# Performance work log

Measured on AMD Instinct MI355X. Metric: run time of the kernel, lower is better.

The kernel has to match this reference:

```python
import jax, jax.numpy as jnp
import numpy as np

# Problem dimensions (match init_kwargs / input_specs)
B, NT = 4, 256          # shots, timesteps
NZ, NX = 384, 384       # domain
NREC = 128              # receivers
DT, DH = 0.001, 10.0    # time step [s], grid spacing [m]


def setup_inputs() -> dict:
    key = jax.random.key(0)
    k1, k2, k3, k4, k5, k6 = jax.random.split(key, 6)
    # source wavelets, one per shot: [B, NT]
    x = jax.random.normal(k1, (B, NT), dtype=jnp.float32)
    # velocity model 1500..3500 m/s: [NZ, NX]
    vp = 1500.0 + 2000.0 * jax.random.uniform(k2, (NZ, NX), dtype=jnp.float32)
    # per-shot source locations (kept away from the boundary)
    src_y = jax.random.randint(k3, (B,), 20, NZ - 20, dtype=jnp.int32)
    src_x = jax.random.randint(k4, (B,), 20, NX - 20, dtype=jnp.int32)
    # shared receiver array
    rec_y = jax.random.randint(k5, (NREC,), 20, NZ - 20, dtype=jnp.int32)
    rec_x = jax.random.randint(k6, (NREC,), 20, NX - 20, dtype=jnp.int32)
    return {"x": x, "vp": vp, "src_y": src_y, "src_x": src_x,
            "rec_y": rec_y, "rec_x": rec_x}


def _laplacian(u, inv_dh2):
    # 5-point stencil with zero (Dirichlet) boundaries; u: [B, NZ, NX]
    l = (u[:, 2:, 1:-1] + u[:, :-2, 1:-1]
         + u[:, 1:-1, 2:] + u[:, 1:-1, :-2]
         - 4.0 * u[:, 1:-1, 1:-1]) * inv_dh2
    return jnp.pad(l, ((0, 0), (1, 1), (1, 1)))


def reference(x, vp, src_y, src_x, rec_y, rec_x):
    """Second-order acoustic wave time-stepping with scatter source injection
    and receiver gather, as in WaveRNN.forward. Returns [NT, B, NREC] traces."""
    c2dt2 = (vp * DT) ** 2            # [NZ, NX], broadcast over shots
    inv_dh2 = jnp.float32(1.0 / (DH * DH))
    bidx = jnp.arange(B)

    def step(carry, xt):
        h1, h2 = carry                # current / previous wavefields [B,NZ,NX]
        hn = 2.0 * h1 - h2 + c2dt2 * _laplacian(h1, inv_dh2)
        hn = hn.at[bidx, src_y, src_x].add(xt)   # source injection (smask scatter)
        rec = hn[:, rec_y, rec_x]                 # receiver gather [B, NREC]
        return (hn, h1), rec

    h0 = jnp.zeros((B, NZ, NX), dtype=x.dtype)
    (_, _), y = jax.lax.scan(jax.checkpoint(step), (h0, h0), x.T)  # scan over time
    return y  # [NT, B, NREC]
```

## Files before the change

kernel.cpp:

```cpp
#include <hip/hip_runtime.h>

#define BB 4
#define NT 256
#define NZ 384
#define NX 384
#define NREC 128
#define NZX (NZ*NX)
#define BNZX (BB*NZX)
#define DT 0.001f
#define INV_DH2 0.01f

#define TILE 48
#define HALO 8
#define REGN 64
#define NBLK 256
#define NTHR 512
#define FSTRIDE 16

__global__ void wave_init(unsigned* flags) {
    int i = blockIdx.x * blockDim.x + threadIdx.x;
    if (i < NBLK * FSTRIDE) flags[i] = 0u;
}

__device__ inline float dpp_shl1(float v) {
    return __int_as_float(__builtin_amdgcn_update_dpp(
        0, __float_as_int(v), 0x130 , 0xf, 0xf, true));
}
__device__ inline float dpp_shr1(float v) {
    return __int_as_float(__builtin_amdgcn_update_dpp(
        0, __float_as_int(v), 0x138 , 0xf, 0xf, true));
}

__device__ inline void grid_sync(unsigned* flags, unsigned gen, int nbId) {
    __syncthreads();
    if (threadIdx.x < 64) {
        if (threadIdx.x == 0)
            __hip_atomic_store(&flags[blockIdx.x * FSTRIDE], gen,
                               __ATOMIC_RELAXED, __HIP_MEMORY_SCOPE_AGENT);
        for (;;) {
            unsigned f = __hip_atomic_load(&flags[nbId * FSTRIDE],
                             __ATOMIC_RELAXED, __HIP_MEMORY_SCOPE_AGENT);
            if (__all(f >= gen)) break;
            __builtin_amdgcn_s_sleep(1);
        }
    }
    __syncthreads();
}

__global__ __launch_bounds__(NTHR)
void wave_tiled(float* __restrict__ ws, const float* __restrict__ vp,
                const float* __restrict__ x,
                const int* __restrict__ src_y, const int* __restrict__ src_x,
                const int* __restrict__ rec_y, const int* __restrict__ rec_x,
                float* __restrict__ y) {
    __shared__ float bnd[2][16][REGN];
    __shared__ float recBuf[NREC][8];
    __shared__ float xs[NT];
    __shared__ int recLoc[NREC], recOut[NREC];
    __shared__ int recCnt;

    unsigned* flags = (unsigned*)(ws + 4*BNZX);

    const int tid = threadIdx.x;
    const int col = tid & 63;
    const int w   = tid >> 6;
    const int r0  = w << 3;
    const int blk = blockIdx.x;
    const int b  = blk >> 6;
    const int tz = (blk >> 3) & 7;
    const int tx = blk & 7;
    const int oz = tz*TILE - HALO, ox = tx*TILE - HALO;
    const int gx = ox + col;
    const int sy = src_y[b], sx = src_x[b];

    if (tid == 0) recCnt = 0;
    for (int k = tid; k < 16*REGN; k += NTHR) ((float*)bnd[0])[k] = 0.f;
    for (int k = tid; k < NT; k += NTHR) xs[k] = x[b*NT + k];
    __syncthreads();
    for (int r = tid; r < NREC; r += NTHR) {
        int ry = rec_y[r], rx = rec_x[r];
        if (ry/TILE == tz && rx/TILE == tx) {
            int p = atomicAdd(&recCnt, 1);
            recLoc[p] = ((ry - oz) << 6) | (rx - ox);
            recOut[p] = b*NREC + r;
        }
    }
    __syncthreads();

    int myN = 0, myM[4], myP[4];
    bool ovf = false;
    for (int p = 0; p < recCnt; ++p) {
        int rl = recLoc[p];
        if ((rl & 63) == col) {
            int rm = (rl >> 6) - r0;
            if ((unsigned)rm < 8u) {
                if (myN < 4) { myM[myN] = rm; myP[myN] = p; ++myN; }
                else ovf = true;
            }
        }
    }

    int nbId = blk;
    if (tid < 8) {
        int d = tid + (tid >= 4);
        int nz2 = tz + d/3 - 1, nx2 = tx + d%3 - 1;
        if ((unsigned)nz2 < 8u && (unsigned)nx2 < 8u)
            nbId = (b << 6) | (nz2 << 3) | nx2;
    }

    float cur[8], prv[8], c2i[8];
    #pragma unroll
    for (int m = 0; m < 8; ++m) {
        cur[m] = 0.f; prv[m] = 0.f;
        const int gz = oz + r0 + m;
        const bool inner = (gz > 0 && gz < NZ-1 && gx > 0 && gx < NX-1);
        const float v = inner ? vp[gz*NX + gx] * DT : 0.f;
        c2i[m] = v * v * INV_DH2;
    }
    const bool srcCol = (gx == sx);
    const int  srcM   = sy - oz - r0;
    const int  iuUp   = (2*w-1 < 0) ? 0 : 2*w-1;
    const int  iuDn   = (2*w+2 > 15) ? 15 : 2*w+2;
    __syncthreads();

    #pragma unroll 1
    for (int t = 0; t < NT; ++t) {
        const int pr = t & 1, pw = pr ^ 1;
        const float upB = bnd[pr][iuUp][col];
        const float dnB = bnd[pr][iuDn][col];

        float hn[8];
        #pragma unroll
        for (int m = 0; m < 8; ++m) {
            const float ce = cur[m];
            const float up = (m == 0) ? upB : cur[m-1];
            const float dn = (m == 7) ? dnB : cur[m+1];
            const float lf = dpp_shl1(ce);
            const float rt = dpp_shr1(ce);
            const float s  = (up + dn) + (lf + rt);
            hn[m] = fmaf(2.f, ce, -prv[m]) + c2i[m] * fmaf(-4.f, ce, s);
        }
        #pragma unroll
        for (int m = 0; m < 8; ++m) { prv[m] = cur[m]; cur[m] = hn[m]; }

        if (srcCol && (unsigned)srcM < 8u) {
            const float xv = xs[t];
            #pragma unroll
            for (int m = 0; m < 8; ++m) if (m == srcM) cur[m] += xv;
        }
        {
            const int s2 = t & 7;
            if (ovf) {
                for (int p = 0; p < recCnt; ++p) {
                    int rl = recLoc[p];
                    if ((rl & 63) == col) {
                        int rm = (rl >> 6) - r0;
                        if ((unsigned)rm < 8u) {
                            float v = cur[0];
                            #pragma unroll
                            for (int m = 1; m < 8; ++m) if (rm == m) v = cur[m];
                            recBuf[p][s2] = v;
                        }
                    }
                }
            } else {
                #pragma unroll
                for (int k = 0; k < 4; ++k) {
                    if (k < myN) {
                        float v = cur[0];
                        #pragma unroll
                        for (int m = 1; m < 8; ++m) if (myM[k] == m) v = cur[m];
                        recBuf[myP[k]][s2] = v;
                    }
                }
            }
        }
        bnd[pw][2*w  ][col] = cur[0];
        bnd[pw][2*w+1][col] = cur[7];

        if ((t & 7) == 7) {
            const int o = t >> 3;
            __syncthreads();
            for (int k = tid; k < recCnt*8; k += NTHR) {
                int p = k >> 3, s2 = k & 7;
                y[(size_t)((o<<3)+s2)*(BB*NREC) + recOut[p]] = recBuf[p][s2];
            }
            if (t < NT-1) {
                float* Gc = ws + (size_t)(o & 1) * 2*BNZX;
                float* Gp = Gc + BNZX;
                const bool colF = (col >= HALO   && col < REGN-HALO);
                const bool colM = (col >= 2*HALO && col < REGN-2*HALO);
                #pragma unroll
                for (int m = 0; m < 8; ++m) {
                    const int i = r0 + m;
                    const bool rowF = (i >= HALO   && i < REGN-HALO);
                    const bool rowM = (i >= 2*HALO && i < REGN-2*HALO);
                    if (colF && rowF && !(colM && rowM)) {
                        const size_t g = (size_t)b*NZX + (size_t)(oz+i)*NX + gx;
                        __hip_atomic_store(&Gc[g], cur[m],
                                           __ATOMIC_RELAXED, __HIP_MEMORY_SCOPE_AGENT);
                        __hip_atomic_store(&Gp[g], prv[m],
                                           __ATOMIC_RELAXED, __HIP_MEMORY_SCOPE_AGENT);
                    }
                }
                grid_sync(flags, (unsigned)(o + 1), nbId);
                const bool colH = (col < HALO || col >= REGN-HALO);
                const bool gxIn = (gx >= 0 && gx < NX);
                #pragma unroll
                for (int m = 0; m < 8; ++m) {
                    const int i = r0 + m;
                    if (colH || i < HALO || i >= REGN-HALO) {
                        const int gz = oz + i;
                        if (gxIn && gz >= 0 && gz < NZ) {
                            const size_t g = (size_t)b*NZX + (size_t)gz*NX + gx;
                            cur[m] = __hip_atomic_load(&Gc[g],
                                         __ATOMIC_RELAXED, __HIP_MEMORY_SCOPE_AGENT);
                            prv[m] = __hip_atomic_load(&Gp[g],
                                         __ATOMIC_RELAXED, __HIP_MEMORY_SCOPE_AGENT);
                        } else { cur[m] = 0.f; prv[m] = 0.f; }
                    }
                }
                bnd[pw][2*w  ][col] = cur[0];
                bnd[pw][2*w+1][col] = cur[7];
            }
        }
        __syncthreads();
    }
}

extern "C" void kernel_launch(void* const* d_in, const int* in_sizes, int n_in,
                              void* d_out, int out_size, void* d_ws, size_t ws_size,
                              hipStream_t stream) {
    const float* x     = (const float*)d_in[0];
    const float* vp    = (const float*)d_in[1];
    const int*   src_y = (const int*)d_in[2];
    const int*   src_x = (const int*)d_in[3];
    const int*   rec_y = (const int*)d_in[4];
    const int*   rec_x = (const int*)d_in[5];
    float* y  = (float*)d_out;
    float* ws = (float*)d_ws;

    wave_init<<<(NBLK*FSTRIDE + 255)/256, 256, 0, stream>>>((unsigned*)(ws + 4*BNZX));
    wave_tiled<<<NBLK, NTHR, 0, stream>>>(ws, vp, x, src_y, src_x, rec_y, rec_x, y);
}
```

Before: 273.0 us.

## Use 16-step halo with 32-wide tiles to halve grid syncs, pack cur/prv

Widens the halo to 16 and shrinks tile interiors to 32, so 576 blocks (12x12 tiles per shot) exchange halos and grid-sync every 16 steps instead of every 8. The edge warps skip their stencil work once their rows are stale within each 16-step window. The cur/prv pair is packed into one 64-bit atomic store/load, and launch bounds now request 6 blocks per CU. This cuts the number of global barriers and halo transactions in exchange for more blocks, more redundant halo computation, and a requirement that all 576 blocks be co-resident.

```diff
diff --git a/kernel.cpp b/kernel.cpp
--- a/kernel.cpp
+++ b/kernel.cpp
@@ -10,10 +10,12 @@
 #define DT 0.001f
 #define INV_DH2 0.01f
 
-#define TILE 48
-#define HALO 8
+#define TILE 32
+#define HALO 16
 #define REGN 64
-#define NBLK 256
+#define NTD  12
+#define TPB  144
+#define NBLK 576
 #define NTHR 512
 #define FSTRIDE 16
 
@@ -29,6 +31,13 @@
 __device__ inline float dpp_shr1(float v) {
     return __int_as_float(__builtin_amdgcn_update_dpp(
         0, __float_as_int(v), 0x138 , 0xf, 0xf, true));
+}
+
+__device__ inline unsigned long long pk2(float a, float b) {
+    union { float f[2]; unsigned long long u; } t; t.f[0] = a; t.f[1] = b; return t.u;
+}
+__device__ inline void upk2(unsigned long long v, float& a, float& b) {
+    union { unsigned long long u; float f[2]; } t; t.u = v; a = t.f[0]; b = t.f[1];
 }
 
 __device__ inline void grid_sync(unsigned* flags, unsigned gen, int nbId) {
@@ -47,7 +56,7 @@
     __syncthreads();
 }
 
-__global__ __launch_bounds__(NTHR)
+__global__ __launch_bounds__(NTHR, 6)
 void wave_tiled(float* __restrict__ ws, const float* __restrict__ vp,
                 const float* __restrict__ x,
                 const int* __restrict__ src_y, const int* __restrict__ src_x,
@@ -66,9 +75,10 @@
     const int w   = tid >> 6;
     const int r0  = w << 3;
     const int blk = blockIdx.x;
-    const int b  = blk >> 6;
-    const int tz = (blk >> 3) & 7;
-    const int tx = blk & 7;
+    const int b   = blk / TPB;
+    const int rem = blk - b*TPB;
+    const int tz  = rem / NTD;
+    const int tx  = rem - tz*NTD;
     const int oz = tz*TILE - HALO, ox = tx*TILE - HALO;
     const int gx = ox + col;
     const int sy = src_y[b], sx = src_x[b];
@@ -104,8 +114,8 @@
     if (tid < 8) {
         int d = tid + (tid >= 4);
         int nz2 = tz + d/3 - 1, nx2 = tx + d%3 - 1;
-        if ((unsigned)nz2 < 8u && (unsigned)nx2 < 8u)
-            nbId = (b << 6) | (nz2 << 3) | nx2;
+        if ((unsigned)nz2 < (unsigned)NTD && (unsigned)nx2 < (unsigned)NTD)
+            nbId = b*TPB + nz2*NTD + nx2;
     }
 
     float cur[8], prv[8], c2i[8];
@@ -121,108 +131,109 @@
     const int  srcM   = sy - oz - r0;
     const int  iuUp   = (2*w-1 < 0) ? 0 : 2*w-1;
     const int  iuDn   = (2*w+2 > 15) ? 15 : 2*w+2;
+    const bool edgeW = (w == 0) || (w == 7);
     __syncthreads();
 
     #pragma unroll 1
     for (int t = 0; t < NT; ++t) {
         const int pr = t & 1, pw = pr ^ 1;
-        const float upB = bnd[pr][iuUp][col];
-        const float dnB = bnd[pr][iuDn][col];
-
-        float hn[8];
-        #pragma unroll
-        for (int m = 0; m < 8; ++m) {
-            const float ce = cur[m];
-            const float up = (m == 0) ? upB : cur[m-1];
-            const float dn = (m == 7) ? dnB : cur[m+1];
-            const float lf = dpp_shl1(ce);
-            const float rt = dpp_shr1(ce);
-            const float s  = (up + dn) + (lf + rt);
-            hn[m] = fmaf(2.f, ce, -prv[m]) + c2i[m] * fmaf(-4.f, ce, s);
-        }
-        #pragma unroll
-        for (int m = 0; m < 8; ++m) { prv[m] = cur[m]; cur[m] = hn[m]; }
-
-        if (srcCol && (unsigned)srcM < 8u) {
-            const float xv = xs[t];
-            #pragma unroll
-            for (int m = 0; m < 8; ++m) if (m == srcM) cur[m] += xv;
-        }
-        {
-            const int s2 = t & 7;
-            if (ovf) {
-                for (int p = 0; p < recCnt; ++p) {
-                    int rl = recLoc[p];
-                    if ((rl & 63) == col) {
-                        int rm = (rl >> 6) - r0;
-                        if ((unsigned)rm < 8u) {
+        const bool act = !(edgeW && (t & 15) >= 7);
+
+        if (act) {
+            const float upB = bnd[pr][iuUp][col];
+            const float dnB = bnd[pr][iuDn][col];
+
+            float hn[8];
+            #pragma unroll
+            for (int m = 0; m < 8; ++m) {
+                const float ce = cur[m];
+                const float up = (m == 0) ? upB : cur[m-1];
+                const float dn = (m == 7) ? dnB : cur[m+1];
+                const float lf = dpp_shl1(ce);
+                const float rt = dpp_shr1(ce);
+                const float s  = (up + dn) + (lf + rt);
+                hn[m] = fmaf(2.f, ce, -prv[m]) + c2i[m] * fmaf(-4.f, ce, s);
+            }
+            #pragma unroll
+            for (int m = 0; m < 8; ++m) { prv[m] = cur[m]; cur[m] = hn[m]; }
+
+            if (srcCol && (unsigned)srcM < 8u) {
+                const float xv = xs[t];
+                #pragma unroll
+                for (int m = 0; m < 8; ++m) if (m == srcM) cur[m] += xv;
+            }
+            {
+                const int s2 = t & 7;
+                if (ovf) {
+                    for (int p = 0; p < recCnt; ++p) {
+                        int rl = recLoc[p];
+                        if ((rl & 63) == col) {
+                            int rm = (rl >> 6) - r0;
+                            if ((unsigned)rm < 8u) {
+                                float v = cur[0];
+                                #pragma unroll
+                                for (int m = 1; m < 8; ++m) if (rm == m) v = cur[m];
+                                recBuf[p][s2] = v;
+                            }
+                        }
+                    }
+                } else {
+                    #pragma unroll
+                    for (int k = 0; k < 4; ++k) {
+                        if (k < myN) {
                             float v = cur[0];
                             #pragma unroll
-                            for (int m = 1; m < 8; ++m) if (rm == m) v = cur[m];
-                            recBuf[p][s2] = v;
+                            for (int m = 1; m < 8; ++m) if (myM[k] == m) v = cur[m];
+                            recBuf[myP[k]][s2] = v;
                         }
                     }
                 }
-            } else {
-                #pragma unroll
-                for (int k = 0; k < 4; ++k) {
-                    if (k < myN) {
-                        float v = cur[0];
-                        #pragma unroll
-                        for (int m = 1; m < 8; ++m) if (myM[k] == m) v = cur[m];
-                        recBuf[myP[k]][s2] = v;
-                    }
-                }
-            }
-        }
-        bnd[pw][2*w  ][col] = cur[0];
-        bnd[pw][2*w+1][col] = cur[7];
+            }
+            bnd[pw][2*w  ][col] = cur[0];
+            bnd[pw][2*w+1][col] = cur[7];
+        }
 
         if ((t & 7) == 7) {
-            const int o = t >> 3;
+            const int o8 = t >> 3;
             __syncthreads();
             for (int k = tid; k < recCnt*8; k += NTHR) {
                 int p = k >> 3, s2 = k & 7;
-                y[(size_t)((o<<3)+s2)*(BB*NREC) + recOut[p]] = recBuf[p][s2];
-            }
-            if (t < NT-1) {
-                float* Gc = ws + (size_t)(o & 1) * 2*BNZX;
-                float* Gp = Gc + BNZX;
-                const bool colF = (col >= HALO   && col < REGN-HALO);
-                const bool colM = (col >= 2*HALO && col < REGN-2*HALO);
-                #pragma unroll
-                for (int m = 0; m < 8; ++m) {
-                    const int i = r0 + m;
-                    const bool rowF = (i >= HALO   && i < REGN-HALO);
-                    const bool rowM = (i >= 2*HALO && i < REGN-2*HALO);
-                    if (colF && rowF && !(colM && rowM)) {
-                        const size_t g = (size_t)b*NZX + (size_t)(oz+i)*NX + gx;
-                        __hip_atomic_store(&Gc[g], cur[m],
-                                           __ATOMIC_RELAXED, __HIP_MEMORY_SCOPE_AGENT);
-                        __hip_atomic_store(&Gp[g], prv[m],
-                                           __ATOMIC_RELAXED, __HIP_MEMORY_SCOPE_AGENT);
-                    }
+                y[(size_t)((o8<<3)+s2)*(BB*NREC) + recOut[p]] = recBuf[p][s2];
+            }
+        }
+
+        if ((t & 15) == 15 && t < NT-1) {
+            const int o16 = t >> 4;
+            unsigned long long* G = (unsigned long long*)ws
+                                  + (size_t)(o16 & 1) * BNZX;
+            const bool colF = (col >= HALO && col < REGN-HALO);
+            #pragma unroll
+            for (int m = 0; m < 8; ++m) {
+                const int i = r0 + m;
+                if (colF && i >= HALO && i < REGN-HALO) {
+                    const size_t g = (size_t)b*NZX + (size_t)(oz+i)*NX + gx;
+                    __hip_atomic_store(&G[g], pk2(cur[m], prv[m]),
+                                       __ATOMIC_RELAXED, __HIP_MEMORY_SCOPE_AGENT);
                 }
-                grid_sync(flags, (unsigned)(o + 1), nbId);
-                const bool colH = (col < HALO || col >= REGN-HALO);
-                const bool gxIn = (gx >= 0 && gx < NX);
-                #pragma unroll
-                for (int m = 0; m < 8; ++m) {
-                    const int i = r0 + m;
-                    if (colH || i < HALO || i >= REGN-HALO) {
-                        const int gz = oz + i;
-                        if (gxIn && gz >= 0 && gz < NZ) {
-                            const size_t g = (size_t)b*NZX + (size_t)gz*NX + gx;
-                            cur[m] = __hip_atomic_load(&Gc[g],
-                                         __ATOMIC_RELAXED, __HIP_MEMORY_SCOPE_AGENT);
-                            prv[m] = __hip_atomic_load(&Gp[g],
-                                         __ATOMIC_RELAXED, __HIP_MEMORY_SCOPE_AGENT);
-                        } else { cur[m] = 0.f; prv[m] = 0.f; }
-                    }
+            }
+            grid_sync(flags, (unsigned)(o16 + 1), nbId);
+            const bool colH = (col < HALO || col >= REGN-HALO);
+            const bool gxIn = (gx >= 0 && gx < NX);
+            #pragma unroll
+            for (int m = 0; m < 8; ++m) {
+                const int i = r0 + m;
+                if (colH || i < HALO || i >= REGN-HALO) {
+                    const int gz = oz + i;
+                    if (gxIn && gz >= 0 && gz < NZ) {
+                        unsigned long long v = __hip_atomic_load(
+                            &G[(size_t)b*NZX + (size_t)gz*NX + gx],
+                            __ATOMIC_RELAXED, __HIP_MEMORY_SCOPE_AGENT);
+                        upk2(v, cur[m], prv[m]);
+                    } else { cur[m] = 0.f; prv[m] = 0.f; }
                 }
-                bnd[pw][2*w  ][col] = cur[0];
-                bnd[pw][2*w+1][col] = cur[7];
-            }
+            }
+            bnd[pw][2*w  ][col] = cur[0];
+            bnd[pw][2*w+1][col] = cur[7];
         }
         __syncthreads();
     }
```

Result: slower. 399.7 us (+46.4%).

## Interleave two shots per block to hide neighbor halo exchange latency

Applied to the files above, without the earlier changes.

Each block now owns a smaller 24x48 tile for two shots and alternates 4-step half-windows between them. This lets one shot's halo exchange and flag wait overlap with the other shot's compute. The per-window grid sync becomes per-tile flag signalling with split wait/publish points, and the plain syncthreads in the inner step is swapped for a lighter LDS-wait barrier. Halo overhead per tile rises (40 of 64 rows redundant), and the more intricate ordering of flags and shared buffers adds risk of races.

```diff
diff --git a/kernel.cpp b/kernel.cpp
--- a/kernel.cpp
+++ b/kernel.cpp
@@ -10,16 +10,23 @@
 #define DT 0.001f
 #define INV_DH2 0.01f
 
-#define TILE 48
+#define TR 24
+#define TC 48
 #define HALO 8
-#define REGN 64
+#define RR 40
+#define RC 64
+#define NTDR 16
+#define NTDC 8
+#define TPB 128
+#define NTILE 512
 #define NBLK 256
 #define NTHR 512
 #define FSTRIDE 16
+#define NWIN 32
 
 __global__ void wave_init(unsigned* flags) {
     int i = blockIdx.x * blockDim.x + threadIdx.x;
-    if (i < NBLK * FSTRIDE) flags[i] = 0u;
+    if (i < NTILE * FSTRIDE) flags[i] = 0u;
 }
 
 __device__ inline float dpp_shl1(float v) {
@@ -31,20 +38,9 @@
         0, __float_as_int(v), 0x138 , 0xf, 0xf, true));
 }
 
-__device__ inline void grid_sync(unsigned* flags, unsigned gen, int nbId) {
-    __syncthreads();
-    if (threadIdx.x < 64) {
-        if (threadIdx.x == 0)
-            __hip_atomic_store(&flags[blockIdx.x * FSTRIDE], gen,
-                               __ATOMIC_RELAXED, __HIP_MEMORY_SCOPE_AGENT);
-        for (;;) {
-            unsigned f = __hip_atomic_load(&flags[nbId * FSTRIDE],
-                             __ATOMIC_RELAXED, __HIP_MEMORY_SCOPE_AGENT);
-            if (__all(f >= gen)) break;
-            __builtin_amdgcn_s_sleep(1);
-        }
-    }
-    __syncthreads();
+__device__ inline void bar_lds() {
+    asm volatile("s_waitcnt lgkmcnt(0)" ::: "memory");
+    __builtin_amdgcn_s_barrier();
 }
 
 __global__ __launch_bounds__(NTHR)
@@ -53,10 +49,10 @@
                 const int* __restrict__ src_y, const int* __restrict__ src_x,
                 const int* __restrict__ rec_y, const int* __restrict__ rec_x,
                 float* __restrict__ y) {
-    __shared__ float bnd[2][16][REGN];
-    __shared__ float recBuf[NREC][8];
-    __shared__ float xs[NT];
-    __shared__ int recLoc[NREC], recOut[NREC];
+    __shared__ float bnd[2][2][16][RC];
+    __shared__ float recBuf[2*NREC][8];
+    __shared__ float xs[2][NT];
+    __shared__ int recLoc[2*NREC], recOut[2*NREC];
     __shared__ int recCnt;
 
     unsigned* flags = (unsigned*)(ws + 4*BNZX);
@@ -64,25 +60,27 @@
     const int tid = threadIdx.x;
     const int col = tid & 63;
     const int w   = tid >> 6;
-    const int r0  = w << 3;
+    const int r0w = w * 5;
     const int blk = blockIdx.x;
-    const int b  = blk >> 6;
-    const int tz = (blk >> 3) & 7;
-    const int tx = blk & 7;
-    const int oz = tz*TILE - HALO, ox = tx*TILE - HALO;
+    const int pb  = blk >> 7;
+    const int rem = blk & 127;
+    const int tz  = rem >> 3;
+    const int tx  = rem & 7;
+    const int bA = pb, bB = pb + 2;
+    const int oz = tz*TR - HALO, ox = tx*TC - HALO;
     const int gx = ox + col;
-    const int sy = src_y[b], sx = src_x[b];
 
     if (tid == 0) recCnt = 0;
-    for (int k = tid; k < 16*REGN; k += NTHR) ((float*)bnd[0])[k] = 0.f;
-    for (int k = tid; k < NT; k += NTHR) xs[k] = x[b*NT + k];
+    for (int k = tid; k < 2*2*16*RC; k += NTHR) ((float*)bnd)[k] = 0.f;
+    for (int k = tid; k < NT; k += NTHR) { xs[0][k] = x[bA*NT+k]; xs[1][k] = x[bB*NT+k]; }
     __syncthreads();
     for (int r = tid; r < NREC; r += NTHR) {
         int ry = rec_y[r], rx = rec_x[r];
-        if (ry/TILE == tz && rx/TILE == tx) {
-            int p = atomicAdd(&recCnt, 1);
-            recLoc[p] = ((ry - oz) << 6) | (rx - ox);
-            recOut[p] = b*NREC + r;
+        if (ry/TR == tz && rx/TC == tx) {
+            int i = ry - oz, c = rx - ox;
+            int p = atomicAdd(&recCnt, 2);
+            recLoc[p]   = (0<<12) | (i<<6) | c;  recOut[p]   = bA*NREC + r;
+            recLoc[p+1] = (1<<12) | (i<<6) | c;  recOut[p+1] = bB*NREC + r;
         }
     }
     __syncthreads();
@@ -92,139 +90,182 @@
     for (int p = 0; p < recCnt; ++p) {
         int rl = recLoc[p];
         if ((rl & 63) == col) {
-            int rm = (rl >> 6) - r0;
-            if ((unsigned)rm < 8u) {
-                if (myN < 4) { myM[myN] = rm; myP[myN] = p; ++myN; }
+            int rm = ((rl >> 6) & 63) - r0w;
+            if ((unsigned)rm < 5u) {
+                if (myN < 4) { myM[myN] = rm | ((rl>>12)<<3); myP[myN] = p; ++myN; }
                 else ovf = true;
             }
         }
     }
 
-    int nbId = blk;
+    const int tIdx0 = (bA<<7) | rem;
+    int nb0 = tIdx0;
     if (tid < 8) {
         int d = tid + (tid >= 4);
         int nz2 = tz + d/3 - 1, nx2 = tx + d%3 - 1;
-        if ((unsigned)nz2 < 8u && (unsigned)nx2 < 8u)
-            nbId = (b << 6) | (nz2 << 3) | nx2;
-    }
-
-    float cur[8], prv[8], c2i[8];
+        if ((unsigned)nz2 < (unsigned)NTDR && (unsigned)nx2 < (unsigned)NTDC)
+            nb0 = (bA<<7) | (nz2<<3) | nx2;
+    }
+    const int nb1 = nb0 + 2*TPB;
+
+    float cur0[5], prv0[5], cur1[5], prv1[5], c2i[5];
     #pragma unroll
-    for (int m = 0; m < 8; ++m) {
-        cur[m] = 0.f; prv[m] = 0.f;
-        const int gz = oz + r0 + m;
-        const bool inner = (gz > 0 && gz < NZ-1 && gx > 0 && gx < NX-1);
-        const float v = inner ? vp[gz*NX + gx] * DT : 0.f;
-        c2i[m] = v * v * INV_DH2;
-    }
-    const bool srcCol = (gx == sx);
-    const int  srcM   = sy - oz - r0;
-    const int  iuUp   = (2*w-1 < 0) ? 0 : 2*w-1;
-    const int  iuDn   = (2*w+2 > 15) ? 15 : 2*w+2;
+    for (int m = 0; m < 5; ++m) {
+        cur0[m]=prv0[m]=cur1[m]=prv1[m]=0.f;
+        const int gz = oz + r0w + m;
+        const bool inner = (gz>0 && gz<NZ-1 && gx>0 && gx<NX-1);
+        const float v = inner ? vp[gz*NX+gx]*DT : 0.f;
+        c2i[m] = v*v*INV_DH2;
+    }
+    const int sy0=src_y[bA], sx0=src_x[bA], sy1=src_y[bB], sx1=src_x[bB];
+    const bool srcC0 = (gx==sx0), srcC1 = (gx==sx1);
+    const int  sm0 = sy0-oz-r0w, sm1 = sy1-oz-r0w;
+    const int  iuUp = (2*w-1<0)?0:2*w-1, iuDn = (2*w+2>15)?15:2*w+2;
     __syncthreads();
 
-    #pragma unroll 1
-    for (int t = 0; t < NT; ++t) {
-        const int pr = t & 1, pw = pr ^ 1;
-        const float upB = bnd[pr][iuUp][col];
-        const float dnB = bnd[pr][iuDn][col];
-
-        float hn[8];
-        #pragma unroll
-        for (int m = 0; m < 8; ++m) {
-            const float ce = cur[m];
-            const float up = (m == 0) ? upB : cur[m-1];
-            const float dn = (m == 7) ? dnB : cur[m+1];
-            const float lf = dpp_shl1(ce);
-            const float rt = dpp_shr1(ce);
-            const float s  = (up + dn) + (lf + rt);
-            hn[m] = fmaf(2.f, ce, -prv[m]) + c2i[m] * fmaf(-4.f, ce, s);
-        }
-        #pragma unroll
-        for (int m = 0; m < 8; ++m) { prv[m] = cur[m]; cur[m] = hn[m]; }
-
-        if (srcCol && (unsigned)srcM < 8u) {
-            const float xv = xs[t];
+    auto win4 = [&](float (&cur)[5], float (&prv)[5],
+                    float (&bt)[2][16][RC], const float* xsT,
+                    bool srcC, int srcM, int tb, int o, int s0) {
+        #pragma unroll 1
+        for (int s = s0; s < s0+4; ++s) {
+            const int pr = s & 1, pw = pr ^ 1;
+            const float upB = bt[pr][iuUp][col];
+            const float dnB = bt[pr][iuDn][col];
+            float hn[5];
             #pragma unroll
-            for (int m = 0; m < 8; ++m) if (m == srcM) cur[m] += xv;
-        }
-        {
-            const int s2 = t & 7;
+            for (int m = 0; m < 5; ++m) {
+                const float ce = cur[m];
+                const float up = (m==0)? upB : cur[m-1];
+                const float dn = (m==4)? dnB : cur[m+1];
+                const float lf = dpp_shl1(ce);
+                const float rt = dpp_shr1(ce);
+                const float su = (up+dn)+(lf+rt);
+                hn[m] = fmaf(2.f, ce, -prv[m]) + c2i[m]*fmaf(-4.f, ce, su);
+            }
+            #pragma unroll
+            for (int m = 0; m < 5; ++m) { prv[m]=cur[m]; cur[m]=hn[m]; }
+            if (srcC && (unsigned)srcM < 5u) {
+                const float xv = xsT[8*o+s];
+                #pragma unroll
+                for (int m = 0; m < 5; ++m) if (m==srcM) cur[m]+=xv;
+            }
             if (ovf) {
                 for (int p = 0; p < recCnt; ++p) {
                     int rl = recLoc[p];
-                    if ((rl & 63) == col) {
-                        int rm = (rl >> 6) - r0;
-                        if ((unsigned)rm < 8u) {
+                    if ((rl>>12)==tb && (rl&63)==col) {
+                        int rm = ((rl>>6)&63) - r0w;
+                        if ((unsigned)rm<5u) {
                             float v = cur[0];
                             #pragma unroll
-                            for (int m = 1; m < 8; ++m) if (rm == m) v = cur[m];
-                            recBuf[p][s2] = v;
+                            for (int m=1;m<5;++m) if (rm==m) v=cur[m];
+                            recBuf[p][s] = v;
                         }
                     }
                 }
             } else {
                 #pragma unroll
-                for (int k = 0; k < 4; ++k) {
-                    if (k < myN) {
-                        float v = cur[0];
-                        #pragma unroll
-                        for (int m = 1; m < 8; ++m) if (myM[k] == m) v = cur[m];
-                        recBuf[myP[k]][s2] = v;
-                    }
+                for (int k=0;k<4;++k) if (k<myN && (myM[k]>>3)==tb) {
+                    int rm = myM[k]&7;
+                    float v = cur[0];
+                    #pragma unroll
+                    for (int m=1;m<5;++m) if (rm==m) v=cur[m];
+                    recBuf[myP[k]][s] = v;
                 }
             }
-        }
-        bnd[pw][2*w  ][col] = cur[0];
-        bnd[pw][2*w+1][col] = cur[7];
-
-        if ((t & 7) == 7) {
-            const int o = t >> 3;
+            bt[pw][2*w  ][col] = cur[0];
+            bt[pw][2*w+1][col] = cur[4];
+            bar_lds();
+        }
+    };
+
+    auto storeRing = [&](float (&cur)[5], float (&prv)[5], int b, int par) {
+        float* Gc = ws + (size_t)par*2*BNZX;
+        float* Gp = Gc + BNZX;
+        #pragma unroll
+        for (int m = 0; m < 5; ++m) {
+            const int i = r0w + m;
+            const bool ring = (i>=HALO && i<RR-HALO && col>=HALO && col<RC-HALO)
+                          && !(i>=2*HALO && i<RR-2*HALO && col>=2*HALO && col<RC-2*HALO);
+            if (ring) {
+                const size_t g = (size_t)b*NZX + (size_t)(oz+i)*NX + gx;
+                __hip_atomic_store(&Gc[g], cur[m], __ATOMIC_RELAXED, __HIP_MEMORY_SCOPE_AGENT);
+                __hip_atomic_store(&Gp[g], prv[m], __ATOMIC_RELAXED, __HIP_MEMORY_SCOPE_AGENT);
+            }
+        }
+    };
+
+    auto loadHalo = [&](float (&cur)[5], float (&prv)[5], int b, int par) {
+        const float* Gc = ws + (size_t)par*2*BNZX;
+        const float* Gp = Gc + BNZX;
+        const bool colH = (col < HALO || col >= RC-HALO);
+        const bool gxIn = (gx >= 0 && gx < NX);
+        #pragma unroll
+        for (int m = 0; m < 5; ++m) {
+            const int i = r0w + m;
+            if (colH || i < HALO || i >= RR-HALO) {
+                const int gz = oz + i;
+                if (gxIn && gz >= 0 && gz < NZ) {
+                    const size_t g = (size_t)b*NZX + (size_t)gz*NX + gx;
+                    cur[m] = __hip_atomic_load(&Gc[g], __ATOMIC_RELAXED, __HIP_MEMORY_SCOPE_AGENT);
+                    prv[m] = __hip_atomic_load(&Gp[g], __ATOMIC_RELAXED, __HIP_MEMORY_SCOPE_AGENT);
+                } else { cur[m]=0.f; prv[m]=0.f; }
+            }
+        }
+    };
+
+    auto waitF = [&](int nb, unsigned gen) {
+        if (tid < 64) {
+            for (;;) {
+                unsigned f = __hip_atomic_load(&flags[nb*FSTRIDE],
+                                 __ATOMIC_RELAXED, __HIP_MEMORY_SCOPE_AGENT);
+                if (__all(f >= gen)) break;
+                __builtin_amdgcn_s_sleep(1);
+            }
+        }
+    };
+
+    #pragma unroll 1
+    for (int o = 0; o < NWIN; ++o) {
+        if (o > 0) {
+            waitF(nb1, (unsigned)o);
+            bar_lds();
+            loadHalo(cur1, prv1, bB, (o-1)&1);
+        }
+        win4(cur0, prv0, bnd[0], xs[0], srcC0, sm0, 0, o, 0);
+        win4(cur0, prv0, bnd[0], xs[0], srcC0, sm0, 0, o, 4);
+        if (o > 0) {
+            bnd[1][0][2*w  ][col] = cur1[0];
+            bnd[1][0][2*w+1][col] = cur1[4];
+        }
+        const bool ex = (o < NWIN-1);
+        if (ex) storeRing(cur0, prv0, bA, o&1);
+        bar_lds();
+        win4(cur1, prv1, bnd[1], xs[1], srcC1, sm1, 1, o, 0);
+        if (ex) {
             __syncthreads();
-            for (int k = tid; k < recCnt*8; k += NTHR) {
-                int p = k >> 3, s2 = k & 7;
-                y[(size_t)((o<<3)+s2)*(BB*NREC) + recOut[p]] = recBuf[p][s2];
-            }
-            if (t < NT-1) {
-                float* Gc = ws + (size_t)(o & 1) * 2*BNZX;
-                float* Gp = Gc + BNZX;
-                const bool colF = (col >= HALO   && col < REGN-HALO);
-                const bool colM = (col >= 2*HALO && col < REGN-2*HALO);
-                #pragma unroll
-                for (int m = 0; m < 8; ++m) {
-                    const int i = r0 + m;
-                    const bool rowF = (i >= HALO   && i < REGN-HALO);
-                    const bool rowM = (i >= 2*HALO && i < REGN-2*HALO);
-                    if (colF && rowF && !(colM && rowM)) {
-                        const size_t g = (size_t)b*NZX + (size_t)(oz+i)*NX + gx;
-                        __hip_atomic_store(&Gc[g], cur[m],
-                                           __ATOMIC_RELAXED, __HIP_MEMORY_SCOPE_AGENT);
-                        __hip_atomic_store(&Gp[g], prv[m],
-                                           __ATOMIC_RELAXED, __HIP_MEMORY_SCOPE_AGENT);
-                    }
-                }
-                grid_sync(flags, (unsigned)(o + 1), nbId);
-                const bool colH = (col < HALO || col >= REGN-HALO);
-                const bool gxIn = (gx >= 0 && gx < NX);
-                #pragma unroll
-                for (int m = 0; m < 8; ++m) {
-                    const int i = r0 + m;
-                    if (colH || i < HALO || i >= REGN-HALO) {
-                        const int gz = oz + i;
-                        if (gxIn && gz >= 0 && gz < NZ) {
-                            const size_t g = (size_t)b*NZX + (size_t)gz*NX + gx;
-                            cur[m] = __hip_atomic_load(&Gc[g],
-                                         __ATOMIC_RELAXED, __HIP_MEMORY_SCOPE_AGENT);
-                            prv[m] = __hip_atomic_load(&Gp[g],
-                                         __ATOMIC_RELAXED, __HIP_MEMORY_SCOPE_AGENT);
-                        } else { cur[m] = 0.f; prv[m] = 0.f; }
-                    }
-                }
-                bnd[pw][2*w  ][col] = cur[0];
-                bnd[pw][2*w+1][col] = cur[7];
-            }
-        }
-        __syncthreads();
+            if (tid == 0)
+                __hip_atomic_store(&flags[tIdx0*FSTRIDE], (unsigned)(o+1),
+                                   __ATOMIC_RELAXED, __HIP_MEMORY_SCOPE_AGENT);
+            waitF(nb0, (unsigned)(o+1));
+            bar_lds();
+            loadHalo(cur0, prv0, bA, o&1);
+        }
+        win4(cur1, prv1, bnd[1], xs[1], srcC1, sm1, 1, o, 4);
+        if (ex) {
+            bnd[0][0][2*w  ][col] = cur0[0];
+            bnd[0][0][2*w+1][col] = cur0[4];
+            storeRing(cur1, prv1, bB, o&1);
+        }
+        for (int k = tid; k < recCnt*8; k += NTHR) {
+            int p = k >> 3, s2 = k & 7;
+            y[(size_t)((o<<3)+s2)*(BB*NREC) + recOut[p]] = recBuf[p][s2];
+        }
+        if (ex) {
+            __syncthreads();
+            if (tid == 0)
+                __hip_atomic_store(&flags[(tIdx0 + 2*TPB)*FSTRIDE], (unsigned)(o+1),
+                                   __ATOMIC_RELAXED, __HIP_MEMORY_SCOPE_AGENT);
+        }
     }
 }
 
@@ -240,6 +281,6 @@
     float* y  = (float*)d_out;
     float* ws = (float*)d_ws;
 
-    wave_init<<<(NBLK*FSTRIDE + 255)/256, 256, 0, stream>>>((unsigned*)(ws + 4*BNZX));
+    wave_init<<<(NTILE*FSTRIDE + 255)/256, 256, 0, stream>>>((unsigned*)(ws + 4*BNZX));
     wave_tiled<<<NBLK, NTHR, 0, stream>>>(ws, vp, x, src_y, src_x, rec_y, rec_x, y);
 }
```

Measured after the change: 406.3 us. 1.49x slower.
